# Performance work log

Measured on AMD Instinct MI355X. Metric: run time of the kernel, lower is better.

## Reference

```python
import jax, jax.numpy as jnp
import numpy as np

B, N, DIM, H = 1, 512, 384, 8
SK, SV, PK, PV = 16, 16, 4, 4
PAIR = 128
EPS = 1e-8


def _rand_rotations(key, b, n):
    m = jax.random.normal(key, (b, n, 3, 3), dtype=jnp.float32)
    q, _ = jnp.linalg.qr(m)  # orthonormal frames
    return q


def setup_inputs() -> dict:
    key = jax.random.key(0)
    ks = jax.random.split(key, 16)
    w = lambda k, shape: jax.random.normal(k, shape, dtype=jnp.float32) * 0.02
    inp = {
        "x": jax.random.normal(ks[0], (B, N, DIM), dtype=jnp.float32),
        "pairwise_repr": jax.random.normal(ks[1], (B, N, N, PAIR), dtype=jnp.float32),
        "rotations": _rand_rotations(ks[2], B, N),
        "translations": jax.random.normal(ks[3], (B, N, 3), dtype=jnp.float32),
        "W_sq": w(ks[4], (DIM, H * SK)),
        "W_sk": w(ks[5], (DIM, H * SK)),
        "W_sv": w(ks[6], (DIM, H * SV)),
        "W_pq": w(ks[7], (DIM, H * PK * 3)),
        "W_pk": w(ks[8], (DIM, H * PK * 3)),
        "W_pv": w(ks[9], (DIM, H * PV * 3)),
        "W_pair": w(ks[10], (PAIR, H)),
        "b_pair": jnp.zeros((H,), dtype=jnp.float32),
        # softplus(point_weights) == 1 at init, per the original log(e-1) init
        "point_weights": jnp.full((H,), float(np.log(np.e - 1.0)), dtype=jnp.float32),
        "W_out": w(ks[11], (H * (SV + PV * 3 + PV + PAIR), DIM)),
        "b_out": jnp.zeros((DIM,), dtype=jnp.float32),
    }
    return inp


def reference(x, pairwise_repr, rotations, translations,
              W_sq, W_sk, W_sv, W_pq, W_pk, W_pv,
              W_pair, b_pair, point_weights, W_out, b_out):
    b, n, _ = x.shape
    scalar_scale = (3 * SK) ** -0.5          # 3 logit terms
    point_scale = ((3 * PK) * (9.0 / 2.0)) ** -0.5
    pair_scale = 3.0 ** -0.5

    q_s = (x @ W_sq).reshape(b, n, H, SK)
    k_s = (x @ W_sk).reshape(b, n, H, SK)
    v_s = (x @ W_sv).reshape(b, n, H, SV)

    def to_global_points(W, d):
        p = (x @ W).reshape(b, n, H, d, 3)           # local-frame points
        p = jnp.einsum('bnhdc,bncr->bnhdr', p, rotations)
        return p + translations[:, :, None, None, :]  # global frame

    q_p = to_global_points(W_pq, PK)
    k_p = to_global_points(W_pk, PK)
    v_p = to_global_points(W_pv, PV)

    # scalar attention logits
    logits = jnp.einsum('bihd,bjhd->bhij', q_s, k_s) * scalar_scale
    # pairwise bias logits
    pair_bias = jnp.einsum('bijp,ph->bhij', pairwise_repr, W_pair) + b_pair[None, :, None, None]
    logits = logits + pair_bias * pair_scale
    # point-distance logits
    diff = q_p[:, :, None] - k_p[:, None]            # (b, i, j, h, d, 3)
    dist2 = jnp.sum(diff * diff, axis=(-1, -2))      # (b, i, j, h)
    pw = jax.nn.softplus(point_weights)              # (h,)
    logits = logits - 0.5 * point_scale * jnp.transpose(dist2, (0, 3, 1, 2)) * pw[None, :, None, None]

    attn = jax.nn.softmax(logits, axis=-1)           # (b, h, i, j)

    out_s = jnp.einsum('bhij,bjhd->bihd', attn, v_s).reshape(b, n, H * SV)
    out_pair = jnp.einsum('bhij,bijp->bihp', attn, pairwise_repr).reshape(b, n, H * PAIR)
    pts = jnp.einsum('bhij,bjhdc->bihdc', attn, v_p)  # global-frame value points
    # rotate back to local frame with R^T
    pts_local = jnp.einsum('bihdc,bicr->bihdr',
                           pts - translations[:, :, None, None, :],
                           jnp.swapaxes(rotations, -1, -2))
    pts_norm = jnp.sqrt(jnp.sum(pts_local ** 2, axis=-1) + EPS)

    feats = jnp.concatenate([
        out_s,
        pts_local.reshape(b, n, H * PV * 3),
        pts_norm.reshape(b, n, H * PV),
        out_pair,
    ], axis=-1)
    return feats @ W_out + b_out
```

## Files before the change

kernel.cpp:

```cpp
#include <hip/hip_runtime.h>
#include <hip/hip_bf16.h>
#include <math.h>

#define NN 512
#define DIMX 384
#define HH 8
#define PAIRD 128

#define SCALAR_SCALE 0.144337567297406f
#define POINT_SCALE  0.136082763487954f
#define PAIR_SCALE   0.577350269189626f

#define KSL 8
#define KPER 160

__global__ __launch_bounds__(256) void k_proj_gemm(
    const float* __restrict__ x,
    const float* __restrict__ Wsq, const float* __restrict__ Wsk, const float* __restrict__ Wsv,
    const float* __restrict__ Wpq, const float* __restrict__ Wpk, const float* __restrict__ Wpv,
    float* __restrict__ qs, float* __restrict__ ks, float* __restrict__ vs,
    float* __restrict__ plq, float* __restrict__ plk, float* __restrict__ plv)
{
    const int m0 = blockIdx.x * 64;
    const int t  = blockIdx.y;
    int ldw, c0;
    const float* W;
    float* out;
    if (t < 12) {
        const float* Ws[3] = {Wsq, Wsk, Wsv};
        float* outs[3] = {qs, ks, vs};
        W = Ws[t >> 2]; out = outs[t >> 2]; c0 = (t & 3) * 32; ldw = 128;
    } else {
        const int u = t - 12;
        const float* Wp[3] = {Wpq, Wpk, Wpv};
        float* outp[3] = {plq, plk, plv};
        W = Wp[u / 3]; out = outp[u / 3]; c0 = (u % 3) * 32; ldw = 96;
    }
    const int tid = threadIdx.x;
    __shared__ float xs[32][68];
    __shared__ float Bs[32][36];
    const int tx = tid & 15, ty = tid >> 4;
    float acc[4][2] = {};

    for (int kt = 0; kt < DIMX; kt += 32) {
        #pragma unroll
        for (int it = 0; it < 2; ++it) {
            int l = tid + it * 256;
            int row = l >> 3, kq = l & 7;
            float4 a = *(const float4*)&x[(size_t)(m0 + row) * DIMX + kt + kq * 4];
            xs[kq*4+0][row] = a.x; xs[kq*4+1][row] = a.y;
            xs[kq*4+2][row] = a.z; xs[kq*4+3][row] = a.w;
        }
        {
            int kk = tid >> 3, nq = tid & 7;
            float4 b = *(const float4*)&W[(size_t)(kt + kk) * ldw + c0 + nq * 4];
            *(float4*)&Bs[kk][nq * 4] = b;
        }
        __syncthreads();
        #pragma unroll
        for (int k = 0; k < 32; ++k) {
            float4 a  = *(const float4*)&xs[k][ty * 4];
            float2 bv = *(const float2*)&Bs[k][tx * 2];
            acc[0][0] += a.x * bv.x; acc[0][1] += a.x * bv.y;
            acc[1][0] += a.y * bv.x; acc[1][1] += a.y * bv.y;
            acc[2][0] += a.z * bv.x; acc[2][1] += a.z * bv.y;
            acc[3][0] += a.w * bv.x; acc[3][1] += a.w * bv.y;
        }
        __syncthreads();
    }
    #pragma unroll
    for (int r = 0; r < 4; ++r) {
        float2 v = make_float2(acc[r][0], acc[r][1]);
        *(float2*)&out[(size_t)(m0 + ty * 4 + r) * ldw + c0 + tx * 2] = v;
    }
}

__global__ __launch_bounds__(256) void k_frames(
    const float* __restrict__ plq, const float* __restrict__ plk, const float* __restrict__ plv,
    const float* __restrict__ rot, const float* __restrict__ trans,
    float* __restrict__ qp, float* __restrict__ kp, float* __restrict__ vp)
{
    int g = blockIdx.x * 256 + threadIdx.x;
    int m = g >> 14;
    int rem = g & 16383;
    int i = rem >> 5;
    int p = rem & 31;
    const float* pl = (m == 0 ? plq : (m == 1 ? plk : plv));
    float*       o  = (m == 0 ? qp  : (m == 1 ? kp  : vp));
    const float* l = &pl[(size_t)i * 96 + p * 3];
    const float* R = &rot[(size_t)i * 9];
    const float* T = &trans[(size_t)i * 3];
    float l0 = l[0], l1 = l[1], l2 = l[2];
    float* op = o + (size_t)i * 96 + p * 3;
    #pragma unroll
    for (int c = 0; c < 3; ++c)
        op[c] = l0 * R[0 * 3 + c] + l1 * R[1 * 3 + c] + l2 * R[2 * 3 + c] + T[c];
}

__global__ __launch_bounds__(256) void k_attn(
    const float* __restrict__ pair,
    const float* __restrict__ qs, const float* __restrict__ ks,
    const float* __restrict__ qp, const float* __restrict__ kp,
    const float* __restrict__ vs, const float* __restrict__ vp,
    const float* __restrict__ Wpair, const float* __restrict__ bpair, const float* __restrict__ pwts,
    const float* __restrict__ rot, const float* __restrict__ trans,
    float* __restrict__ feats)
{
    const int i   = blockIdx.x;
    const int tid = threadIdx.x;

    __shared__ float smem[10392];
    float* ptileA = smem;
    float* wpt    = smem + 8448;
    float* wbuf   = smem + 9472;
    float* corrb  = smem + 10048;
    float* qs_s   = smem + 10064;
    float* qp_s   = smem + 10192;
    float* l_s    = smem + 10288;
    float* pts_s  = smem + 10296;
    float4* red4  = (float4*)smem;

    for (int l = tid; l < 1024; l += 256) {
        int hh = l >> 7, p = l & 127;
        wpt[hh * 128 + p] = Wpair[p * 8 + hh];
    }
    if (tid < 32) ((float4*)qs_s)[tid] = ((const float4*)(qs + (size_t)i * 128))[tid];
    if (tid < 24) ((float4*)qp_s)[tid] = ((const float4*)(qp + (size_t)i * 96))[tid];

    const int h  = tid >> 5;
    const int jj = tid & 31;
    const int jg = h;
    const int pq = jj;

    const float bp_h = bpair[h];
    const float pw_h = log1pf(__expf(pwts[h]));

    float m_run = -1e30f, l_run = 0.f;
    float4 accP[8];
    #pragma unroll
    for (int z = 0; z < 8; ++z) accP[z] = make_float4(0, 0, 0, 0);
    float4 accS = make_float4(0, 0, 0, 0);
    float4 accV = make_float4(0, 0, 0, 0);

    const float4* pair4 = (const float4*)(pair + (size_t)i * NN * PAIRD);
    const float4* vs4   = (const float4*)vs;
    const float4* vp4   = (const float4*)vp;

    float4 r0 = pair4[tid], r1 = pair4[tid + 256], r2 = pair4[tid + 512], r3 = pair4[tid + 768];

    for (int t = 0; t < 16; ++t) {
        float* pt = ptileA + (t & 1) * 4224;
        float* wt = wbuf   + (t & 1) * 288;
        float* cb = corrb  + (t & 1) * 8;

        { int l0 = tid;       *(float4*)&pt[(l0 >> 5) * 132 + (l0 & 31) * 4] = r0; }
        { int l1 = tid + 256; *(float4*)&pt[(l1 >> 5) * 132 + (l1 & 31) * 4] = r1; }
        { int l2 = tid + 512; *(float4*)&pt[(l2 >> 5) * 132 + (l2 & 31) * 4] = r2; }
        { int l3 = tid + 768; *(float4*)&pt[(l3 >> 5) * 132 + (l3 & 31) * 4] = r3; }
        __syncthreads();

        if (t < 15) {
            const float4* psn = pair4 + (size_t)(t + 1) * 1024;
            r0 = psn[tid]; r1 = psn[tid + 256]; r2 = psn[tid + 512]; r3 = psn[tid + 768];
        }

        const int j = t * 32 + jj;
        float bias = 0.f;
        {
            const float4* prow = (const float4*)&pt[jj * 132];
            const float4* wrow = (const float4*)&wpt[h * 128];
            #pragma unroll 8
            for (int p4 = 0; p4 < 32; ++p4) {
                float4 a = prow[p4], w = wrow[p4];
                bias += a.x * w.x + a.y * w.y + a.z * w.z + a.w * w.w;
            }
        }
        float sc = 0.f;
        {
            const float4* kr4 = (const float4*)(ks + (size_t)j * 128 + h * 16);
            const float4* qr4 = (const float4*)&qs_s[h * 16];
            #pragma unroll
            for (int q = 0; q < 4; ++q) {
                float4 kq = kr4[q], qq = qr4[q];
                sc += qq.x * kq.x + qq.y * kq.y + qq.z * kq.z + qq.w * kq.w;
            }
        }
        float d2 = 0.f;
        {
            const float4* kp4 = (const float4*)(kp + (size_t)j * 96 + h * 12);
            const float4* qp4 = (const float4*)&qp_s[h * 12];
            #pragma unroll
            for (int q = 0; q < 3; ++q) {
                float4 kq = kp4[q], qq = qp4[q];
                float dx = qq.x - kq.x, dy = qq.y - kq.y, dz = qq.z - kq.z, dw = qq.w - kq.w;
                d2 += dx * dx + dy * dy + dz * dz + dw * dw;
            }
        }
        float lg = sc * SCALAR_SCALE + (bias + bp_h) * PAIR_SCALE
                 - 0.5f * POINT_SCALE * pw_h * d2;

        float tm = lg;
        #pragma unroll
        for (int off = 16; off > 0; off >>= 1) tm = fmaxf(tm, __shfl_xor(tm, off));
        float m_new = fmaxf(m_run, tm);
        float corr  = __expf(m_run - m_new);
        float p     = __expf(lg - m_new);
        float ps    = p;
        #pragma unroll
        for (int off = 16; off > 0; off >>= 1) ps += __shfl_xor(ps, off);
        l_run = l_run * corr + ps;
        m_run = m_new;
        wt[h * 36 + jj] = p;
        if (jj == 0) cb[h] = corr;
        __syncthreads();

        #pragma unroll
        for (int z = 0; z < 8; ++z) {
            float c = cb[z];
            accP[z].x *= c; accP[z].y *= c; accP[z].z *= c; accP[z].w *= c;
        }
        {
            float c = cb[pq >> 2];
            accS.x *= c; accS.y *= c; accS.z *= c; accS.w *= c;
        }
        if (pq < 24) {
            float c = cb[pq / 3];
            accV.x *= c; accV.y *= c; accV.z *= c; accV.w *= c;
        }
        #pragma unroll
        for (int jo = 0; jo < 4; ++jo) {
            const int jl = jo * 8 + jg;
            float4 pr = *(const float4*)&pt[jl * 132 + pq * 4];
            #pragma unroll
            for (int z = 0; z < 8; ++z) {
                float a = wt[z * 36 + jl];
                accP[z].x += a * pr.x; accP[z].y += a * pr.y;
                accP[z].z += a * pr.z; accP[z].w += a * pr.w;
            }
            {
                float a = wt[(pq >> 2) * 36 + jl];
                float4 v = vs4[(size_t)(t * 32 + jl) * 32 + pq];
                accS.x += a * v.x; accS.y += a * v.y; accS.z += a * v.z; accS.w += a * v.w;
            }
            if (pq < 24) {
                float a = wt[(pq / 3) * 36 + jl];
                float4 v = vp4[(size_t)(t * 32 + jl) * 24 + pq];
                accV.x += a * v.x; accV.y += a * v.y; accV.z += a * v.z; accV.w += a * v.w;
            }
        }
    }

    if (jj == 0) l_s[h] = l_run;
    __syncthreads();

    #pragma unroll
    for (int z = 0; z < 8; ++z) red4[(jg * 8 + z) * 32 + pq] = accP[z];
    __syncthreads();
    {
        const int ho = tid >> 5, p4 = tid & 31;
        float4 s = red4[ho * 32 + p4];
        #pragma unroll
        for (int g = 1; g < 8; ++g) {
            float4 v = red4[(g * 8 + ho) * 32 + p4];
            s.x += v.x; s.y += v.y; s.z += v.z; s.w += v.w;
        }
        float inv = 1.f / l_s[ho];
        s.x *= inv; s.y *= inv; s.z *= inv; s.w *= inv;
        ((float4*)&feats[(size_t)i * 1280 + 256])[tid] = s;
    }
    __syncthreads();

    red4[jg * 32 + pq] = accS;
    if (pq < 24) red4[256 + jg * 24 + pq] = accV;
    __syncthreads();
    if (tid < 32) {
        float4 s = red4[tid];
        #pragma unroll
        for (int g = 1; g < 8; ++g) {
            float4 v = red4[g * 32 + tid];
            s.x += v.x; s.y += v.y; s.z += v.z; s.w += v.w;
        }
        float inv = 1.f / l_s[tid >> 2];
        s.x *= inv; s.y *= inv; s.z *= inv; s.w *= inv;
        ((float4*)&feats[(size_t)i * 1280])[tid] = s;
    } else if (tid < 56) {
        const int pc = tid - 32;
        float4 s = red4[256 + pc];
        #pragma unroll
        for (int g = 1; g < 8; ++g) {
            float4 v = red4[256 + g * 24 + pc];
            s.x += v.x; s.y += v.y; s.z += v.z; s.w += v.w;
        }
        float inv = 1.f / l_s[pc / 3];
        s.x *= inv; s.y *= inv; s.z *= inv; s.w *= inv;
        ((float4*)pts_s)[pc] = s;
    }
    __syncthreads();

    if (tid < 32) {
        const float* R = &rot[(size_t)i * 9];
        const float* T = &trans[(size_t)i * 3];
        float px = pts_s[tid * 3 + 0] - T[0];
        float py = pts_s[tid * 3 + 1] - T[1];
        float pz = pts_s[tid * 3 + 2] - T[2];
        float n2 = 0.f;
        float* fo = feats + (size_t)i * 1280;
        #pragma unroll
        for (int r = 0; r < 3; ++r) {
            float lr = px * R[r * 3 + 0] + py * R[r * 3 + 1] + pz * R[r * 3 + 2];
            fo[128 + tid * 3 + r] = lr;
            n2 += lr * lr;
        }
        fo[224 + tid] = sqrtf(n2 + 1e-8f);
    }
}

__global__ __launch_bounds__(256) void k_final_gemm(
    const float* __restrict__ feats, const float* __restrict__ Wout,
    float* __restrict__ partial)
{
    const int m0 = blockIdx.x * 128;
    const int n0 = blockIdx.y * 128;
    const int ks = blockIdx.z;
    const int tid = threadIdx.x;
    const int k0 = ks * KPER;
    __shared__ float As[16][132];
    __shared__ float Bs[16][132];
    const int tx = tid & 15, ty = tid >> 4;
    float acc[8][8] = {};

    for (int kt = 0; kt < KPER; kt += 16) {
        #pragma unroll
        for (int it = 0; it < 2; ++it) {
            const int l = tid + it * 256;
            const int row = l >> 2, kq = l & 3;
            float4 a = *(const float4*)&feats[(size_t)(m0 + row) * 1280 + k0 + kt + kq * 4];
            As[kq * 4 + 0][row] = a.x; As[kq * 4 + 1][row] = a.y;
            As[kq * 4 + 2][row] = a.z; As[kq * 4 + 3][row] = a.w;
            const int kk = l >> 5, nq = l & 31;
            float4 b = *(const float4*)&Wout[(size_t)(k0 + kt + kk) * 384 + n0 + nq * 4];
            *(float4*)&Bs[kk][nq * 4] = b;
        }
        __syncthreads();
        #pragma unroll
        for (int k = 0; k < 16; ++k) {
            float4 a0 = *(const float4*)&As[k][ty * 8];
            float4 a1 = *(const float4*)&As[k][ty * 8 + 4];
            float4 b0 = *(const float4*)&Bs[k][tx * 8];
            float4 b1 = *(const float4*)&Bs[k][tx * 8 + 4];
            float am[8] = {a0.x, a0.y, a0.z, a0.w, a1.x, a1.y, a1.z, a1.w};
            float bn[8] = {b0.x, b0.y, b0.z, b0.w, b1.x, b1.y, b1.z, b1.w};
            #pragma unroll
            for (int r = 0; r < 8; ++r)
                #pragma unroll
                for (int c = 0; c < 8; ++c)
                    acc[r][c] += am[r] * bn[c];
        }
        __syncthreads();
    }
    float* po = partial + (size_t)ks * (512 * 384);
    #pragma unroll
    for (int r = 0; r < 8; ++r) {
        *(float4*)&po[(size_t)(m0 + ty * 8 + r) * 384 + n0 + tx * 8]     = *(float4*)&acc[r][0];
        *(float4*)&po[(size_t)(m0 + ty * 8 + r) * 384 + n0 + tx * 8 + 4] = *(float4*)&acc[r][4];
    }
}

__global__ __launch_bounds__(256) void k_reduce(
    const float* __restrict__ partial, const float* __restrict__ bout,
    float* __restrict__ out)
{
    const int f = blockIdx.x * 256 + threadIdx.x;
    const int e = f * 4;
    const int col = e % 384;
    float4 acc = *(const float4*)&bout[col];
    #pragma unroll
    for (int s = 0; s < KSL; ++s) {
        float4 p = *(const float4*)&partial[(size_t)s * (512 * 384) + e];
        acc.x += p.x; acc.y += p.y; acc.z += p.z; acc.w += p.w;
    }
    *(float4*)&out[e] = acc;
}

extern "C" void kernel_launch(void* const* d_in, const int* in_sizes, int n_in,
                              void* d_out, int out_size, void* d_ws, size_t ws_size,
                              hipStream_t stream) {
    const float* x     = (const float*)d_in[0];
    const float* pair  = (const float*)d_in[1];
    const float* rot   = (const float*)d_in[2];
    const float* trans = (const float*)d_in[3];
    const float* Wsq   = (const float*)d_in[4];
    const float* Wsk   = (const float*)d_in[5];
    const float* Wsv   = (const float*)d_in[6];
    const float* Wpq   = (const float*)d_in[7];
    const float* Wpk   = (const float*)d_in[8];
    const float* Wpv   = (const float*)d_in[9];
    const float* Wpair = (const float*)d_in[10];
    const float* bpair = (const float*)d_in[11];
    const float* pwts  = (const float*)d_in[12];
    const float* Wout  = (const float*)d_in[13];
    const float* bout  = (const float*)d_in[14];

    float* ws      = (float*)d_ws;
    float* qs      = ws;
    float* ks      = qs + 512 * 128;
    float* vs      = ks + 512 * 128;
    float* qp      = vs + 512 * 128;
    float* kp      = qp + 512 * 96;
    float* vp      = kp + 512 * 96;
    float* feats   = vp + 512 * 96;
    float* partial = feats + 512 * 1280;
    float* plq     = partial + KSL * 512 * 384;
    float* plk     = plq + 512 * 96;
    float* plv     = plk + 512 * 96;

    k_proj_gemm<<<dim3(8, 21), 256, 0, stream>>>(x, Wsq, Wsk, Wsv, Wpq, Wpk, Wpv,
                                                 qs, ks, vs, plq, plk, plv);
    k_frames<<<192, 256, 0, stream>>>(plq, plk, plv, rot, trans, qp, kp, vp);
    k_attn<<<512, 256, 0, stream>>>(pair, qs, ks, qp, kp, vs, vp,
                                    Wpair, bpair, pwts, rot, trans, feats);
    k_final_gemm<<<dim3(4, 3, KSL), 256, 0, stream>>>(feats, Wout, partial);
    k_reduce<<<192, 256, 0, stream>>>(partial, bout, (float*)d_out);
}
```

Baseline: 125.7 us.

## Split attention over key chunks with flash-decoding style merge kernel

Splits each query row's attention over 4 key chunks, launching 2048 blocks instead of 512, and adds a merge kernel that combines the partial max/sum/accumulators with softmax rescaling. The single-buffered tile also cuts shared memory, which should raise occupancy. The pair-bias computation is rebalanced so each thread computes all 8 heads over a slice of channels and reduces them with a shuffle butterfly. The cost is an extra kernel launch and a partial-result buffer round-trip through global memory, which reuses the final GEMM's partial workspace.

```diff
diff --git a/kernel.cpp b/kernel.cpp
--- a/kernel.cpp
+++ b/kernel.cpp
@@ -13,6 +13,7 @@
 
 #define KSL 8
 #define KPER 160
+#define PCH 1264
 
 __global__ __launch_bounds__(256) void k_proj_gemm(
     const float* __restrict__ x,
@@ -102,38 +103,37 @@
     const float* __restrict__ qs, const float* __restrict__ ks,
     const float* __restrict__ qp, const float* __restrict__ kp,
     const float* __restrict__ vs, const float* __restrict__ vp,
-    const float* __restrict__ Wpair, const float* __restrict__ bpair, const float* __restrict__ pwts,
-    const float* __restrict__ rot, const float* __restrict__ trans,
-    float* __restrict__ feats)
+    const float* __restrict__ Wpair, const float* __restrict__ bpair,
+    const float* __restrict__ pwts,
+    float* __restrict__ attnp)
 {
-    const int i   = blockIdx.x;
+    const int jc  = blockIdx.x;
+    const int i   = blockIdx.y;
     const int tid = threadIdx.x;
 
-    __shared__ float smem[10392];
-    float* ptileA = smem;
-    float* wpt    = smem + 8448;
-    float* wbuf   = smem + 9472;
-    float* corrb  = smem + 10048;
-    float* qs_s   = smem + 10064;
-    float* qp_s   = smem + 10192;
-    float* l_s    = smem + 10288;
-    float* pts_s  = smem + 10296;
-    float4* red4  = (float4*)smem;
+    __shared__ float smem[5768];
+    float* pt   = smem;
+    float* wpt  = smem + 4224;
+    float* wt   = smem + 5248;
+    float* cb   = smem + 5536;
+    float* qs_s = smem + 5544;
+    float* qp_s = smem + 5672;
 
     for (int l = tid; l < 1024; l += 256) {
-        int hh = l >> 7, p = l & 127;
-        wpt[hh * 128 + p] = Wpair[p * 8 + hh];
+        float v = Wpair[l];
+        wpt[(l & 7) * 128 + (l >> 3)] = v;
     }
     if (tid < 32) ((float4*)qs_s)[tid] = ((const float4*)(qs + (size_t)i * 128))[tid];
     if (tid < 24) ((float4*)qp_s)[tid] = ((const float4*)(qp + (size_t)i * 96))[tid];
 
-    const int h  = tid >> 5;
-    const int jj = tid & 31;
-    const int jg = h;
-    const int pq = jj;
-
-    const float bp_h = bpair[h];
-    const float pw_h = log1pf(__expf(pwts[h]));
+    const int g   = tid & 7;
+    const int jjL = tid >> 3;
+    const int h2  = tid >> 5;
+    const int jj2 = tid & 31;
+    const int jg  = h2, pq = jj2;
+
+    const float bp_h = bpair[g];
+    const float pw_h = log1pf(__expf(pwts[g]));
 
     float m_run = -1e30f, l_run = 0.f;
     float4 accP[8];
@@ -142,43 +142,59 @@
     float4 accS = make_float4(0, 0, 0, 0);
     float4 accV = make_float4(0, 0, 0, 0);
 
-    const float4* pair4 = (const float4*)(pair + (size_t)i * NN * PAIRD);
+    const float4* pair4 = (const float4*)(pair + ((size_t)i * NN + jc * 128) * PAIRD);
     const float4* vs4   = (const float4*)vs;
     const float4* vp4   = (const float4*)vp;
 
     float4 r0 = pair4[tid], r1 = pair4[tid + 256], r2 = pair4[tid + 512], r3 = pair4[tid + 768];
 
-    for (int t = 0; t < 16; ++t) {
-        float* pt = ptileA + (t & 1) * 4224;
-        float* wt = wbuf   + (t & 1) * 288;
-        float* cb = corrb  + (t & 1) * 8;
-
-        { int l0 = tid;       *(float4*)&pt[(l0 >> 5) * 132 + (l0 & 31) * 4] = r0; }
-        { int l1 = tid + 256; *(float4*)&pt[(l1 >> 5) * 132 + (l1 & 31) * 4] = r1; }
-        { int l2 = tid + 512; *(float4*)&pt[(l2 >> 5) * 132 + (l2 & 31) * 4] = r2; }
-        { int l3 = tid + 768; *(float4*)&pt[(l3 >> 5) * 132 + (l3 & 31) * 4] = r3; }
-        __syncthreads();
-
-        if (t < 15) {
-            const float4* psn = pair4 + (size_t)(t + 1) * 1024;
-            r0 = psn[tid]; r1 = psn[tid + 256]; r2 = psn[tid + 512]; r3 = psn[tid + 768];
-        }
-
-        const int j = t * 32 + jj;
-        float bias = 0.f;
+    for (int t = 0; t < 4; ++t) {
+        *(float4*)&pt[(tid >> 5) * 132 + (tid & 31) * 4]         = r0;
+        *(float4*)&pt[((tid + 256) >> 5) * 132 + (tid & 31) * 4] = r1;
+        *(float4*)&pt[((tid + 512) >> 5) * 132 + (tid & 31) * 4] = r2;
+        *(float4*)&pt[((tid + 768) >> 5) * 132 + (tid & 31) * 4] = r3;
+        __syncthreads();
+
+        if (t < 3) {
+            const float4* nx = pair4 + (size_t)(t + 1) * 1024;
+            r0 = nx[tid]; r1 = nx[tid + 256]; r2 = nx[tid + 512]; r3 = nx[tid + 768];
+        }
+
+        float b[8] = {0,0,0,0,0,0,0,0};
+        #pragma unroll
+        for (int q = 0; q < 4; ++q) {
+            float4 a = *(const float4*)&pt[jjL * 132 + q * 32 + g * 4];
+            #pragma unroll
+            for (int z = 0; z < 8; ++z) {
+                float4 w = *(const float4*)&wpt[z * 128 + q * 32 + g * 4];
+                b[z] += a.x * w.x + a.y * w.y + a.z * w.z + a.w * w.w;
+            }
+        }
+        float v0, v1, v2, v3, w0, w1, bias;
         {
-            const float4* prow = (const float4*)&pt[jj * 132];
-            const float4* wrow = (const float4*)&wpt[h * 128];
-            #pragma unroll 8
-            for (int p4 = 0; p4 < 32; ++p4) {
-                float4 a = prow[p4], w = wrow[p4];
-                bias += a.x * w.x + a.y * w.y + a.z * w.z + a.w * w.w;
-            }
-        }
+            float o0 = __shfl_xor(b[0], 4), o1 = __shfl_xor(b[1], 4);
+            float o2 = __shfl_xor(b[2], 4), o3 = __shfl_xor(b[3], 4);
+            float o4 = __shfl_xor(b[4], 4), o5 = __shfl_xor(b[5], 4);
+            float o6 = __shfl_xor(b[6], 4), o7 = __shfl_xor(b[7], 4);
+            bool s2 = (g & 4);
+            v0 = s2 ? (b[4] + o4) : (b[0] + o0);
+            v1 = s2 ? (b[5] + o5) : (b[1] + o1);
+            v2 = s2 ? (b[6] + o6) : (b[2] + o2);
+            v3 = s2 ? (b[7] + o7) : (b[3] + o3);
+            float p0 = __shfl_xor(v0, 2), p1 = __shfl_xor(v1, 2);
+            float p2 = __shfl_xor(v2, 2), p3 = __shfl_xor(v3, 2);
+            bool s1 = (g & 2);
+            w0 = s1 ? (v2 + p2) : (v0 + p0);
+            w1 = s1 ? (v3 + p3) : (v1 + p1);
+            float q0 = __shfl_xor(w0, 1), q1 = __shfl_xor(w1, 1);
+            bias = (g & 1) ? (w1 + q1) : (w0 + q0);
+        }
+
+        const int j = jc * 128 + t * 32 + jjL;
         float sc = 0.f;
         {
-            const float4* kr4 = (const float4*)(ks + (size_t)j * 128 + h * 16);
-            const float4* qr4 = (const float4*)&qs_s[h * 16];
+            const float4* kr4 = (const float4*)(ks + (size_t)j * 128 + g * 16);
+            const float4* qr4 = (const float4*)&qs_s[g * 16];
             #pragma unroll
             for (int q = 0; q < 4; ++q) {
                 float4 kq = kr4[q], qq = qr4[q];
@@ -187,8 +203,8 @@
         }
         float d2 = 0.f;
         {
-            const float4* kp4 = (const float4*)(kp + (size_t)j * 96 + h * 12);
-            const float4* qp4 = (const float4*)&qp_s[h * 12];
+            const float4* kp4 = (const float4*)(kp + (size_t)j * 96 + g * 12);
+            const float4* qp4 = (const float4*)&qp_s[g * 12];
             #pragma unroll
             for (int q = 0; q < 3; ++q) {
                 float4 kq = kp4[q], qq = qp4[q];
@@ -196,22 +212,26 @@
                 d2 += dx * dx + dy * dy + dz * dz + dw * dw;
             }
         }
-        float lg = sc * SCALAR_SCALE + (bias + bp_h) * PAIR_SCALE
-                 - 0.5f * POINT_SCALE * pw_h * d2;
-
-        float tm = lg;
-        #pragma unroll
-        for (int off = 16; off > 0; off >>= 1) tm = fmaxf(tm, __shfl_xor(tm, off));
-        float m_new = fmaxf(m_run, tm);
-        float corr  = __expf(m_run - m_new);
-        float p     = __expf(lg - m_new);
-        float ps    = p;
-        #pragma unroll
-        for (int off = 16; off > 0; off >>= 1) ps += __shfl_xor(ps, off);
-        l_run = l_run * corr + ps;
-        m_run = m_new;
-        wt[h * 36 + jj] = p;
-        if (jj == 0) cb[h] = corr;
+        wt[g * 36 + jjL] = sc * SCALAR_SCALE + (bias + bp_h) * PAIR_SCALE
+                         - 0.5f * POINT_SCALE * pw_h * d2;
+        __syncthreads();
+
+        {
+            float lg = wt[h2 * 36 + jj2];
+            float tm = lg;
+            #pragma unroll
+            for (int off = 16; off > 0; off >>= 1) tm = fmaxf(tm, __shfl_xor(tm, off));
+            float m_new = fmaxf(m_run, tm);
+            float corr  = __expf(m_run - m_new);
+            float p     = __expf(lg - m_new);
+            float ps    = p;
+            #pragma unroll
+            for (int off = 16; off > 0; off >>= 1) ps += __shfl_xor(ps, off);
+            l_run = l_run * corr + ps;
+            m_run = m_new;
+            wt[h2 * 36 + jj2] = p;
+            if (jj2 == 0) cb[h2] = corr;
+        }
         __syncthreads();
 
         #pragma unroll
@@ -230,6 +250,7 @@
         #pragma unroll
         for (int jo = 0; jo < 4; ++jo) {
             const int jl = jo * 8 + jg;
+            const int jglob = jc * 128 + t * 32 + jl;
             float4 pr = *(const float4*)&pt[jl * 132 + pq * 4];
             #pragma unroll
             for (int z = 0; z < 8; ++z) {
@@ -239,59 +260,139 @@
             }
             {
                 float a = wt[(pq >> 2) * 36 + jl];
-                float4 v = vs4[(size_t)(t * 32 + jl) * 32 + pq];
+                float4 v = vs4[(size_t)jglob * 32 + pq];
                 accS.x += a * v.x; accS.y += a * v.y; accS.z += a * v.z; accS.w += a * v.w;
             }
             if (pq < 24) {
                 float a = wt[(pq / 3) * 36 + jl];
-                float4 v = vp4[(size_t)(t * 32 + jl) * 24 + pq];
+                float4 v = vp4[(size_t)jglob * 24 + pq];
                 accV.x += a * v.x; accV.y += a * v.y; accV.z += a * v.z; accV.w += a * v.w;
             }
         }
-    }
-
-    if (jj == 0) l_s[h] = l_run;
+        __syncthreads();
+    }
+
+    float* attnc = attnp + ((size_t)i * 4 + jc) * PCH;
+    if (jj2 == 0) { attnc[1248 + h2] = m_run; attnc[1256 + h2] = l_run; }
+
+    #pragma unroll
+    for (int z = 0; z < 8; ++z) {
+        accP[z].x += __shfl_xor(accP[z].x, 32); accP[z].y += __shfl_xor(accP[z].y, 32);
+        accP[z].z += __shfl_xor(accP[z].z, 32); accP[z].w += __shfl_xor(accP[z].w, 32);
+    }
+    accS.x += __shfl_xor(accS.x, 32); accS.y += __shfl_xor(accS.y, 32);
+    accS.z += __shfl_xor(accS.z, 32); accS.w += __shfl_xor(accS.w, 32);
+    accV.x += __shfl_xor(accV.x, 32); accV.y += __shfl_xor(accV.y, 32);
+    accV.z += __shfl_xor(accV.z, 32); accV.w += __shfl_xor(accV.w, 32);
+
+    float4* redP = (float4*)smem;
+    float4* redS = (float4*)(smem + 4224);
+    float4* redV = (float4*)(smem + 4736);
+    const int jgp = jg >> 1;
+    if ((jg & 1) == 0) {
+        #pragma unroll
+        for (int z = 0; z < 8; ++z) redP[(jgp * 8 + z) * 32 + pq] = accP[z];
+        redS[jgp * 32 + pq] = accS;
+        if (pq < 24) redV[jgp * 24 + pq] = accV;
+    }
     __syncthreads();
 
-    #pragma unroll
-    for (int z = 0; z < 8; ++z) red4[(jg * 8 + z) * 32 + pq] = accP[z];
+    {
+        const int z = tid >> 5, p4 = tid & 31;
+        float4 s = redP[z * 32 + p4];
+        #pragma unroll
+        for (int gg = 1; gg < 4; ++gg) {
+            float4 v = redP[(gg * 8 + z) * 32 + p4];
+            s.x += v.x; s.y += v.y; s.z += v.z; s.w += v.w;
+        }
+        *(float4*)&attnc[z * 128 + p4 * 4] = s;
+    }
+    if (tid < 32) {
+        float4 s = redS[tid];
+        #pragma unroll
+        for (int gg = 1; gg < 4; ++gg) {
+            float4 v = redS[gg * 32 + tid];
+            s.x += v.x; s.y += v.y; s.z += v.z; s.w += v.w;
+        }
+        *(float4*)&attnc[1024 + tid * 4] = s;
+    } else if (tid < 56) {
+        const int pc = tid - 32;
+        float4 s = redV[pc];
+        #pragma unroll
+        for (int gg = 1; gg < 4; ++gg) {
+            float4 v = redV[gg * 24 + pc];
+            s.x += v.x; s.y += v.y; s.z += v.z; s.w += v.w;
+        }
+        *(float4*)&attnc[1152 + pc * 4] = s;
+    }
+}
+
+__global__ __launch_bounds__(256) void k_attn_merge(
+    const float* __restrict__ attnp,
+    const float* __restrict__ rot, const float* __restrict__ trans,
+    float* __restrict__ feats)
+{
+    const int i = blockIdx.x;
+    const int tid = threadIdx.x;
+    __shared__ float sm_m[32], sm_l[32], sW[32], sL[8], pts_s[96];
+
+    const float* base = attnp + (size_t)i * 4 * PCH;
+    if (tid < 32) {
+        int jcx = tid >> 3, h = tid & 7;
+        sm_m[jcx * 8 + h] = base[jcx * PCH + 1248 + h];
+        sm_l[jcx * 8 + h] = base[jcx * PCH + 1256 + h];
+    }
     __syncthreads();
+    if (tid < 8) {
+        const int h = tid;
+        float M = fmaxf(fmaxf(sm_m[h], sm_m[8 + h]), fmaxf(sm_m[16 + h], sm_m[24 + h]));
+        float L = 0.f;
+        #pragma unroll
+        for (int jcx = 0; jcx < 4; ++jcx) {
+            float w = __expf(sm_m[jcx * 8 + h] - M);
+            L += sm_l[jcx * 8 + h] * w;
+            sW[jcx * 8 + h] = w;
+        }
+        sL[h] = L;
+    }
+    __syncthreads();
+
     {
-        const int ho = tid >> 5, p4 = tid & 31;
-        float4 s = red4[ho * 32 + p4];
-        #pragma unroll
-        for (int g = 1; g < 8; ++g) {
-            float4 v = red4[(g * 8 + ho) * 32 + p4];
-            s.x += v.x; s.y += v.y; s.z += v.z; s.w += v.w;
-        }
-        float inv = 1.f / l_s[ho];
+        const int h = tid >> 5, pq = tid & 31;
+        float4 s = make_float4(0, 0, 0, 0);
+        #pragma unroll
+        for (int jcx = 0; jcx < 4; ++jcx) {
+            float4 a = *(const float4*)&base[jcx * PCH + h * 128 + pq * 4];
+            float w = sW[jcx * 8 + h];
+            s.x += a.x * w; s.y += a.y * w; s.z += a.z * w; s.w += a.w * w;
+        }
+        float inv = 1.f / sL[h];
         s.x *= inv; s.y *= inv; s.z *= inv; s.w *= inv;
         ((float4*)&feats[(size_t)i * 1280 + 256])[tid] = s;
     }
-    __syncthreads();
-
-    red4[jg * 32 + pq] = accS;
-    if (pq < 24) red4[256 + jg * 24 + pq] = accV;
-    __syncthreads();
     if (tid < 32) {
-        float4 s = red4[tid];
-        #pragma unroll
-        for (int g = 1; g < 8; ++g) {
-            float4 v = red4[g * 32 + tid];
-            s.x += v.x; s.y += v.y; s.z += v.z; s.w += v.w;
-        }
-        float inv = 1.f / l_s[tid >> 2];
+        const int h = tid >> 2;
+        float4 s = make_float4(0, 0, 0, 0);
+        #pragma unroll
+        for (int jcx = 0; jcx < 4; ++jcx) {
+            float4 a = *(const float4*)&base[jcx * PCH + 1024 + tid * 4];
+            float w = sW[jcx * 8 + h];
+            s.x += a.x * w; s.y += a.y * w; s.z += a.z * w; s.w += a.w * w;
+        }
+        float inv = 1.f / sL[h];
         s.x *= inv; s.y *= inv; s.z *= inv; s.w *= inv;
         ((float4*)&feats[(size_t)i * 1280])[tid] = s;
     } else if (tid < 56) {
         const int pc = tid - 32;
-        float4 s = red4[256 + pc];
-        #pragma unroll
-        for (int g = 1; g < 8; ++g) {
-            float4 v = red4[256 + g * 24 + pc];
-            s.x += v.x; s.y += v.y; s.z += v.z; s.w += v.w;
-        }
-        float inv = 1.f / l_s[pc / 3];
+        const int h = pc / 3;
+        float4 s = make_float4(0, 0, 0, 0);
+        #pragma unroll
+        for (int jcx = 0; jcx < 4; ++jcx) {
+            float4 a = *(const float4*)&base[jcx * PCH + 1152 + pc * 4];
+            float w = sW[jcx * 8 + h];
+            s.x += a.x * w; s.y += a.y * w; s.z += a.z * w; s.w += a.w * w;
+        }
+        float inv = 1.f / sL[h];
         s.x *= inv; s.y *= inv; s.z *= inv; s.w *= inv;
         ((float4*)pts_s)[pc] = s;
     }
@@ -409,16 +510,18 @@
     float* kp      = qp + 512 * 96;
     float* vp      = kp + 512 * 96;
     float* feats   = vp + 512 * 96;
-    float* partial = feats + 512 * 1280;
-    float* plq     = partial + KSL * 512 * 384;
+    float* attnp   = feats + 512 * 1280;
+    float* partial = attnp;
+    float* plq     = attnp + 2048 * PCH;
     float* plk     = plq + 512 * 96;
     float* plv     = plk + 512 * 96;
 
     k_proj_gemm<<<dim3(8, 21), 256, 0, stream>>>(x, Wsq, Wsk, Wsv, Wpq, Wpk, Wpv,
                                                  qs, ks, vs, plq, plk, plv);
     k_frames<<<192, 256, 0, stream>>>(plq, plk, plv, rot, trans, qp, kp, vp);
-    k_attn<<<512, 256, 0, stream>>>(pair, qs, ks, qp, kp, vs, vp,
-                                    Wpair, bpair, pwts, rot, trans, feats);
+    k_attn<<<dim3(4, 512), 256, 0, stream>>>(pair, qs, ks, qp, kp, vs, vp,
+                                             Wpair, bpair, pwts, attnp);
+    k_attn_merge<<<512, 256, 0, stream>>>(attnp, rot, trans, feats);
     k_final_gemm<<<dim3(4, 3, KSL), 256, 0, stream>>>(feats, Wout, partial);
     k_reduce<<<192, 256, 0, stream>>>(partial, bout, (float*)d_out);
 }
```

Measured after the change: 126.3 us. No clear change (+0.6%).
